# Kernel tuning notes

Hardware: AMD Instinct MI355X
Metric: run time of the kernel (lower is better)

Reference implementation:

```python
import jax, jax.numpy as jnp
import numpy as np


def setup_inputs() -> dict:
    key = jax.random.key(0)
    ks = jax.random.split(key, 9)
    B, L, D, H, E = 8, 2048, 1024, 256, 8
    Hg = D // 4
    s = 0.02
    return {
        "x": jax.random.normal(ks[0], (B, L, D), dtype=jnp.float32),
        "wg1": jax.random.normal(ks[1], (D, Hg), dtype=jnp.float32) * s,
        "bg1": jax.random.normal(ks[2], (Hg,), dtype=jnp.float32) * s,
        "wg2": jax.random.normal(ks[3], (Hg, E), dtype=jnp.float32) * s,
        "bg2": jax.random.normal(ks[4], (E,), dtype=jnp.float32) * s,
        "w1": jax.random.normal(ks[5], (E, D, H), dtype=jnp.float32) * (1.0 / np.sqrt(D)),
        "b1": jax.random.normal(ks[6], (E, H), dtype=jnp.float32) * s,
        "w2": jax.random.normal(ks[7], (E, H, D), dtype=jnp.float32) * (1.0 / np.sqrt(H)),
        "b2": jax.random.normal(ks[8], (E, D), dtype=jnp.float32) * s,
        "k": 2,
    }


def reference(x, wg1, bg1, wg2, bg2, w1, b1, w2, b2, k):
    B, L, D = x.shape
    xt = x.reshape(-1, D)                       # [T, D] tokens
    T = xt.shape[0]
    # gating MLP: Linear -> GELU(exact, matches torch nn.GELU) -> Linear -> softmax
    logits = jax.nn.gelu(xt @ wg1 + bg1, approximate=False) @ wg2 + bg2  # [T, E]
    scores = jax.nn.softmax(logits, axis=-1)
    top_v, top_i = jax.lax.top_k(scores, k)     # [T, k]
    # dense gate matrix (equivalent to compute_gating's scatter); zeros for non-top-k
    gates = jnp.zeros_like(scores).at[jnp.arange(T)[:, None], top_i].set(top_v)  # [T, E]

    # grouped-GEMM MoE: y[t] = sum_e gates[t,e] * (gelu(x[t] @ W1_e + b1_e) @ W2_e + b2_e)
    # scan over the fixed, small expert axis; gates zero out non-selected experts,
    # giving math identical to the sort/dispatch + per-expert torch.mm loop.
    def body(acc, we):
        w1e, b1e, w2e, b2e, ge = we
        h = jax.nn.gelu(xt @ w1e + b1e, approximate=False)  # [T, H]
        o = h @ w2e + b2e                                    # [T, D]
        return acc + ge[:, None] * o, None

    y, _ = jax.lax.scan(body, jnp.zeros_like(xt), (w1, b1, w2, b2, gates.T))
    return y.reshape(B, L, D)
```

## Files before the change

kernel.cpp:

```cpp
#include <hip/hip_runtime.h>

typedef unsigned short u16;
typedef __attribute__((ext_vector_type(8))) short bf16x8;
typedef __attribute__((ext_vector_type(4))) float f32x4;
typedef __attribute__((ext_vector_type(4))) u16 u16x4;

#define T_TOK 16384
#define D_DIM 1024
#define NE 8
#define MAXP 33792

__device__ __forceinline__ u16 f2bf(float f) {
  union { float f; unsigned int u; } c; c.f = f;
  unsigned int u = c.u;
  u += 0x7fffu + ((u >> 16) & 1u);
  return (u16)(u >> 16);
}

__device__ __forceinline__ float bf2f(u16 v) {
  union { unsigned int u; float f; } c; c.u = ((unsigned int)v) << 16;
  return c.f;
}

__device__ __forceinline__ float gelu_exact(float u) {
  return 0.5f * u * (1.0f + erff(u * 0.70710678118654752f));
}

__device__ __forceinline__ void gld16(const void* g, void* l) {
  __builtin_amdgcn_global_load_lds(
      (const __attribute__((address_space(1))) unsigned int*)g,
      (__attribute__((address_space(3))) unsigned int*)l, 16, 0, 0);
}

__device__ __forceinline__ void stage_tile(u16* lds, const char* g0, size_t stride,
                                           int wid, int lane) {
  const char* g = g0 + (size_t)(wid * 8 + (lane >> 3)) * stride + (size_t)((lane & 7) * 16);
  char* l = (char*)lds + wid * 1024;
  #pragma unroll
  for (int c = 0; c < 4; ++c)
    gld16(g + (size_t)(32 * c) * stride, l + c * 4096);
}

__device__ __forceinline__ void stage_b32(u16* lds, const u16* mat, int rowbase,
                                          int k0, int wid, int lane) {
  const char* g0 = (const char*)(mat + (size_t)rowbase * 1024 + k0);
  #pragma unroll
  for (int c = 0; c < 2; ++c) {
    const int row = c * 64 + wid * 16 + (lane >> 2);
    const char* g = g0 + (size_t)row * 2048 + (size_t)((lane & 3) * 16);
    char* l = (char*)lds + c * 4096 + wid * 1024;
    gld16(g, l);
  }
}

__device__ __forceinline__ void mma_step(const u16* As, const u16* Bs, f32x4 acc[4][4],
                                         int wm, int wn, int lane) {
  const int r = lane & 15, kq = (lane >> 4) * 8;
  #pragma unroll
  for (int ks = 0; ks < 2; ++ks) {
    const int col = ks * 32 + kq;
    bf16x8 a[4], b[4];
    #pragma unroll
    for (int mf = 0; mf < 4; ++mf)
      a[mf] = *(const bf16x8*)&As[(wm * 64 + mf * 16 + r) * 64 + col];
    #pragma unroll
    for (int nf = 0; nf < 4; ++nf)
      b[nf] = *(const bf16x8*)&Bs[(wn * 64 + nf * 16 + r) * 64 + col];
    #pragma unroll
    for (int mf = 0; mf < 4; ++mf)
      #pragma unroll
      for (int nf = 0; nf < 4; ++nf)
        acc[mf][nf] = __builtin_amdgcn_mfma_f32_16x16x32_bf16(a[mf], b[nf], acc[mf][nf], 0, 0, 0);
  }
}

__global__ __launch_bounds__(256) void transpose_cvt_kernel(const float* __restrict__ in,
                                                            u16* __restrict__ out,
                                                            int R, int C) {
  __shared__ u16 t[32][36];
  const int e = blockIdx.z;
  const int r0 = blockIdx.x * 32, c0 = blockIdx.y * 32;
  const int tid = threadIdx.x;
  {
    const int r = tid >> 3, cq = (tid & 7) * 4;
    float4 v = *(const float4*)(in + ((size_t)e * R + r0 + r) * C + c0 + cq);
    t[r][cq + 0] = f2bf(v.x); t[r][cq + 1] = f2bf(v.y);
    t[r][cq + 2] = f2bf(v.z); t[r][cq + 3] = f2bf(v.w);
  }
  __syncthreads();
  {
    const int c = tid >> 3, rq = (tid & 7) * 4;
    u16x4 o;
    o.x = t[rq + 0][c]; o.y = t[rq + 1][c]; o.z = t[rq + 2][c]; o.w = t[rq + 3][c];
    *(u16x4*)(out + ((size_t)e * C + c0 + c) * R + r0 + rq) = o;
  }
}

__global__ __launch_bounds__(256) void transpose_hilo_kernel(const float* __restrict__ in,
                                                             u16* __restrict__ out_hi,
                                                             u16* __restrict__ out_lo,
                                                             int R, int C) {
  __shared__ u16 th[32][36];
  __shared__ u16 tl[32][36];
  const int r0 = blockIdx.x * 32, c0 = blockIdx.y * 32;
  const int tid = threadIdx.x;
  {
    const int r = tid >> 3, cq = (tid & 7) * 4;
    float4 v = *(const float4*)(in + (size_t)(r0 + r) * C + c0 + cq);
    float vv[4] = {v.x, v.y, v.z, v.w};
    #pragma unroll
    for (int i = 0; i < 4; ++i) {
      u16 h = f2bf(vv[i]);
      th[r][cq + i] = h;
      tl[r][cq + i] = f2bf(vv[i] - bf2f(h));
    }
  }
  __syncthreads();
  {
    const int c = tid >> 3, rq = (tid & 7) * 4;
    u16x4 oh, ol;
    oh.x = th[rq + 0][c]; oh.y = th[rq + 1][c]; oh.z = th[rq + 2][c]; oh.w = th[rq + 3][c];
    ol.x = tl[rq + 0][c]; ol.y = tl[rq + 1][c]; ol.z = tl[rq + 2][c]; ol.w = tl[rq + 3][c];
    *(u16x4*)(out_hi + (size_t)(c0 + c) * R + r0 + rq) = oh;
    *(u16x4*)(out_lo + (size_t)(c0 + c) * R + r0 + rq) = ol;
  }
}

__global__ __launch_bounds__(256) void gating_mfma_kernel(
    const float* __restrict__ x, const u16* __restrict__ wg1t_hi,
    const u16* __restrict__ wg1t_lo, u16* __restrict__ xb,
    float* __restrict__ p_buf) {
  __shared__ u16 Ah[2][128 * 32], Al[2][128 * 32];
  __shared__ u16 Bh[2][128 * 32], Bl[2][128 * 32];
  const int tid = threadIdx.x, lane = tid & 63, wid = tid >> 6;
  const int t0 = blockIdx.x * 128, n0 = blockIdx.y * 128;
  const int wm = wid >> 1, wn = wid & 1;
  const bool emit = (blockIdx.y == 0);
  const int arow = tid >> 1, akb = (tid & 1) * 16;

  f32x4 acc[4][4];
  #pragma unroll
  for (int i = 0; i < 4; ++i)
    #pragma unroll
    for (int j = 0; j < 4; ++j) acc[i][j] = (f32x4){0.f, 0.f, 0.f, 0.f};

  stage_b32(Bh[0], wg1t_hi, n0, 0, wid, lane);
  stage_b32(Bl[0], wg1t_lo, n0, 0, wid, lane);
  {
    const float* src = x + (size_t)(t0 + arow) * 1024 + akb;
    #pragma unroll
    for (int i = 0; i < 4; ++i) {
      float4 v = *(const float4*)(src + i * 4);
      float vv[4] = {v.x, v.y, v.z, v.w};
      u16x4 h, l;
      u16 hh[4], ll[4];
      #pragma unroll
      for (int q = 0; q < 4; ++q) { hh[q] = f2bf(vv[q]); ll[q] = f2bf(vv[q] - bf2f(hh[q])); }
      h.x = hh[0]; h.y = hh[1]; h.z = hh[2]; h.w = hh[3];
      l.x = ll[0]; l.y = ll[1]; l.z = ll[2]; l.w = ll[3];
      *(u16x4*)&Ah[0][arow * 32 + akb + i * 4] = h;
      *(u16x4*)&Al[0][arow * 32 + akb + i * 4] = l;
      if (emit) *(u16x4*)(xb + (size_t)(t0 + arow) * 1024 + akb + i * 4) = h;
    }
  }
  __syncthreads();

  int cur = 0;
  for (int kt = 0; kt < 32; ++kt) {
    const bool has_next = kt < 31;
    const int nxt = cur ^ 1;
    float4 xv[4];
    if (has_next) {
      stage_b32(Bh[nxt], wg1t_hi, n0, (kt + 1) * 32, wid, lane);
      stage_b32(Bl[nxt], wg1t_lo, n0, (kt + 1) * 32, wid, lane);
      const float* src = x + (size_t)(t0 + arow) * 1024 + (kt + 1) * 32 + akb;
      #pragma unroll
      for (int i = 0; i < 4; ++i) xv[i] = *(const float4*)(src + i * 4);
    }
    {
      const int r = lane & 15, kq = (lane >> 4) * 8;
      bf16x8 ah[4], al[4], bh[4], bl[4];
      #pragma unroll
      for (int mf = 0; mf < 4; ++mf) {
        const int ro = (wm * 64 + mf * 16 + r) * 32 + kq;
        ah[mf] = *(const bf16x8*)&Ah[cur][ro];
        al[mf] = *(const bf16x8*)&Al[cur][ro];
      }
      #pragma unroll
      for (int nf = 0; nf < 4; ++nf) {
        const int ro = (wn * 64 + nf * 16 + r) * 32 + kq;
        bh[nf] = *(const bf16x8*)&Bh[cur][ro];
        bl[nf] = *(const bf16x8*)&Bl[cur][ro];
      }
      #pragma unroll
      for (int mf = 0; mf < 4; ++mf)
        #pragma unroll
        for (int nf = 0; nf < 4; ++nf) {
          acc[mf][nf] = __builtin_amdgcn_mfma_f32_16x16x32_bf16(ah[mf], bh[nf], acc[mf][nf], 0, 0, 0);
          acc[mf][nf] = __builtin_amdgcn_mfma_f32_16x16x32_bf16(ah[mf], bl[nf], acc[mf][nf], 0, 0, 0);
          acc[mf][nf] = __builtin_amdgcn_mfma_f32_16x16x32_bf16(al[mf], bh[nf], acc[mf][nf], 0, 0, 0);
        }
    }
    if (has_next) {
      #pragma unroll
      for (int i = 0; i < 4; ++i) {
        float vv[4] = {xv[i].x, xv[i].y, xv[i].z, xv[i].w};
        u16x4 h, l;
        u16 hh[4], ll[4];
        #pragma unroll
        for (int q = 0; q < 4; ++q) { hh[q] = f2bf(vv[q]); ll[q] = f2bf(vv[q] - bf2f(hh[q])); }
        h.x = hh[0]; h.y = hh[1]; h.z = hh[2]; h.w = hh[3];
        l.x = ll[0]; l.y = ll[1]; l.z = ll[2]; l.w = ll[3];
        *(u16x4*)&Ah[nxt][arow * 32 + akb + i * 4] = h;
        *(u16x4*)&Al[nxt][arow * 32 + akb + i * 4] = l;
        if (emit) *(u16x4*)(xb + (size_t)(t0 + arow) * 1024 + (kt + 1) * 32 + akb + i * 4) = h;
      }
    }
    __syncthreads();
    cur ^= 1;
  }

  #pragma unroll
  for (int mf = 0; mf < 4; ++mf)
    #pragma unroll
    for (int rr = 0; rr < 4; ++rr) {
      const int lt = wm * 64 + mf * 16 + ((lane >> 4) << 2) + rr;
      #pragma unroll
      for (int nf = 0; nf < 4; ++nf) {
        const int ln = wn * 64 + nf * 16 + (lane & 15);
        p_buf[(size_t)(t0 + lt) * 256 + n0 + ln] = acc[mf][nf][rr];
      }
    }
}

__global__ __launch_bounds__(256) void gating_p2_kernel(
    const float* __restrict__ p_buf, const float* __restrict__ bg1,
    const float* __restrict__ wg2, const float* __restrict__ bg2,
    int* __restrict__ top_i, float2* __restrict__ top_g) {
  const int tid = threadIdx.x;
  const int tn = tid & 31, tm = tid >> 5;
  const int t0 = blockIdx.x * 32;

  float bb[8];
  {
    float4 ba = *(const float4*)&bg1[tn * 4];
    float4 bc = *(const float4*)&bg1[128 + tn * 4];
    bb[0] = ba.x; bb[1] = ba.y; bb[2] = ba.z; bb[3] = ba.w;
    bb[4] = bc.x; bb[5] = bc.y; bb[6] = bc.z; bb[7] = bc.w;
  }

  float hv[4][8];
  #pragma unroll
  for (int i = 0; i < 4; ++i) {
    const size_t t = t0 + tm * 4 + i;
    const float* p = &p_buf[t * 256];
    float4 a0 = *(const float4*)&p[tn * 4];
    float4 a1 = *(const float4*)&p[128 + tn * 4];
    hv[i][0] = gelu_exact(a0.x + bb[0]);
    hv[i][1] = gelu_exact(a0.y + bb[1]);
    hv[i][2] = gelu_exact(a0.z + bb[2]);
    hv[i][3] = gelu_exact(a0.w + bb[3]);
    hv[i][4] = gelu_exact(a1.x + bb[4]);
    hv[i][5] = gelu_exact(a1.y + bb[5]);
    hv[i][6] = gelu_exact(a1.z + bb[6]);
    hv[i][7] = gelu_exact(a1.w + bb[7]);
  }

  float part[4][8];
  #pragma unroll
  for (int i = 0; i < 4; ++i)
    #pragma unroll
    for (int e = 0; e < 8; ++e) part[i][e] = 0.f;
  #pragma unroll
  for (int j = 0; j < 8; ++j) {
    const int col = (j < 4) ? (tn * 4 + j) : (128 + tn * 4 + (j - 4));
    float4 wa = *(const float4*)&wg2[col * 8];
    float4 wb = *(const float4*)&wg2[col * 8 + 4];
    float we[8] = {wa.x, wa.y, wa.z, wa.w, wb.x, wb.y, wb.z, wb.w};
    #pragma unroll
    for (int i = 0; i < 4; ++i)
      #pragma unroll
      for (int e = 0; e < 8; ++e) part[i][e] += hv[i][j] * we[e];
  }
  #pragma unroll
  for (int mask = 1; mask < 32; mask <<= 1)
    #pragma unroll
    for (int i = 0; i < 4; ++i)
      #pragma unroll
      for (int e = 0; e < 8; ++e) part[i][e] += __shfl_xor(part[i][e], mask);

  if (tn < 4) {
    float lg[8];
    #pragma unroll
    for (int i = 0; i < 4; ++i)
      if (tn == i) {
        #pragma unroll
        for (int e = 0; e < 8; ++e) lg[e] = part[i][e];
      }
    #pragma unroll
    for (int e = 0; e < 8; ++e) lg[e] += bg2[e];
    float m = lg[0];
    #pragma unroll
    for (int e = 1; e < 8; ++e) m = fmaxf(m, lg[e]);
    float ex[8], s = 0.f;
    #pragma unroll
    for (int e = 0; e < 8; ++e) { ex[e] = expf(lg[e] - m); s += ex[e]; }
    int i1 = 0;
    #pragma unroll
    for (int e = 1; e < 8; ++e) if (lg[e] > lg[i1]) i1 = e;
    int i2 = (i1 == 0) ? 1 : 0;
    #pragma unroll
    for (int e = 0; e < 8; ++e) if (e != i1 && lg[e] > lg[i2]) i2 = e;
    float inv = 1.f / s;
    const int t = t0 + tm * 4 + tn;
    top_i[t] = i1 | (i2 << 8);
    top_g[t] = make_float2(ex[i1] * inv, ex[i2] * inv);
  }
}

__global__ __launch_bounds__(256) void hist_kernel(const int* __restrict__ top_i,
                                                   int* __restrict__ hist) {
  __shared__ int h[NE];
  const int tid = threadIdx.x;
  if (tid < NE) h[tid] = 0;
  __syncthreads();
  const int ti = top_i[blockIdx.x * 256 + tid];
  atomicAdd(&h[ti & 255], 1);
  atomicAdd(&h[ti >> 8], 1);
  __syncthreads();
  if (tid < NE) hist[blockIdx.x * NE + tid] = h[tid];
}

__global__ __launch_bounds__(64) void scan_kernel(const int* __restrict__ hist,
                                                  int* __restrict__ cnt,
                                                  int* __restrict__ offs,
                                                  int* __restrict__ cbase) {
  __shared__ int tot[NE], off_s[NE];
  const int tid = threadIdx.x;
  if (tid < NE) {
    int s = 0;
    for (int c = 0; c < 64; ++c) s += hist[c * NE + tid];
    tot[tid] = s; cnt[tid] = s;
  }
  __syncthreads();
  if (tid == 0) {
    int o = 0;
    #pragma unroll
    for (int e = 0; e < NE; ++e) { off_s[e] = o; o += (tot[e] + 127) & ~127; }
  }
  __syncthreads();
  if (tid < NE) {
    offs[tid] = off_s[tid];
    int r = off_s[tid];
    for (int c = 0; c < 64; ++c) { cbase[c * NE + tid] = r; r += hist[c * NE + tid]; }
  }
}

__global__ __launch_bounds__(256) void fill_kernel(
    const int* __restrict__ top_i, const int* __restrict__ cbase,
    int* __restrict__ tok_list, int* __restrict__ pos1, int* __restrict__ pos2) {
  __shared__ int lcnt[NE];
  const int tid = threadIdx.x;
  if (tid < NE) lcnt[tid] = 0;
  __syncthreads();
  const int t = blockIdx.x * 256 + tid;
  const int ti = top_i[t];
  const int i1 = ti & 255, i2 = ti >> 8;
  const int r1 = atomicAdd(&lcnt[i1], 1);
  const int r2 = atomicAdd(&lcnt[i2], 1);
  const int p1 = cbase[blockIdx.x * NE + i1] + r1;
  const int p2 = cbase[blockIdx.x * NE + i2] + r2;
  tok_list[p1] = t; tok_list[p2] = t;
  pos1[t] = p1; pos2[t] = p2;
}

__global__ __launch_bounds__(256) void expert_h_kernel(
    const u16* __restrict__ xb, const u16* __restrict__ w1t,
    const float* __restrict__ b1, const int* __restrict__ tok_list,
    const int* __restrict__ cnt, const int* __restrict__ offs,
    u16* __restrict__ h_c) {
  __shared__ u16 As[128 * 64];
  __shared__ u16 Bs[128 * 64];
  __shared__ float b1_s[128];
  const int e = blockIdx.z;
  const int nblk = (cnt[e] + 127) >> 7;
  if ((int)blockIdx.x >= nblk) return;
  const int tid = threadIdx.x, lane = tid & 63, wid = tid >> 6;
  const int base = offs[e] + blockIdx.x * 128;
  const int n0 = blockIdx.y * 128;
  const int wm = wid >> 1, wn = wid & 1;

  if (tid < 128) b1_s[tid] = b1[e * 256 + n0 + tid];

  int tk[4];
  {
    const int r0 = wid * 8 + (lane >> 3);
    #pragma unroll
    for (int c = 0; c < 4; ++c) tk[c] = tok_list[base + r0 + 32 * c];
  }

  f32x4 acc[4][4];
  #pragma unroll
  for (int i = 0; i < 4; ++i)
    #pragma unroll
    for (int j = 0; j < 4; ++j) acc[i][j] = (f32x4){0.f, 0.f, 0.f, 0.f};

  const char* Bb = (const char*)w1t + ((size_t)e * 256 + n0) * 2048;
  const int cb = (lane & 7) * 16;
  for (int kt = 0; kt < 16; ++kt) {
    __syncthreads();
    {
      char* l = (char*)As + wid * 1024;
      #pragma unroll
      for (int c = 0; c < 4; ++c)
        gld16((const char*)xb + (size_t)tk[c] * 2048 + kt * 128 + cb, l + c * 4096);
    }
    stage_tile(Bs, Bb + kt * 128, 2048, wid, lane);
    __syncthreads();
    mma_step(As, Bs, acc, wm, wn, lane);
  }

  #pragma unroll
  for (int mf = 0; mf < 4; ++mf)
    #pragma unroll
    for (int rr = 0; rr < 4; ++rr) {
      const int lt = wm * 64 + mf * 16 + ((lane >> 4) << 2) + rr;
      #pragma unroll
      for (int nf = 0; nf < 4; ++nf) {
        const int ln = wn * 64 + nf * 16 + (lane & 15);
        float u = acc[mf][nf][rr] + b1_s[ln];
        h_c[(size_t)(base + lt) * 256 + n0 + ln] = f2bf(gelu_exact(u));
      }
    }
}

__global__ __launch_bounds__(256) void moe_out_kernel(
    const u16* __restrict__ h_c, const u16* __restrict__ w2t,
    const float* __restrict__ b2, const int* __restrict__ cnt,
    const int* __restrict__ offs, u16* __restrict__ o_c) {
  __shared__ u16 As[128 * 64];
  __shared__ u16 Bs[128 * 64];
  __shared__ float b2_s[128];
  const int e = blockIdx.z;
  const int nblk = (cnt[e] + 127) >> 7;
  if ((int)blockIdx.x >= nblk) return;
  const int tid = threadIdx.x, lane = tid & 63, wid = tid >> 6;
  const int base = offs[e] + blockIdx.x * 128;
  const int n0 = blockIdx.y * 128;
  const int wm = wid >> 1, wn = wid & 1;

  if (tid < 128) b2_s[tid] = b2[(size_t)e * 1024 + n0 + tid];

  f32x4 acc[4][4];
  #pragma unroll
  for (int i = 0; i < 4; ++i)
    #pragma unroll
    for (int j = 0; j < 4; ++j) acc[i][j] = (f32x4){0.f, 0.f, 0.f, 0.f};

  const char* Ab = (const char*)h_c + (size_t)base * 512;
  const char* Bb = (const char*)w2t + ((size_t)e * D_DIM + n0) * 512;
  #pragma unroll 1
  for (int kt = 0; kt < 4; ++kt) {
    __syncthreads();
    stage_tile(As, Ab + kt * 128, 512, wid, lane);
    stage_tile(Bs, Bb + kt * 128, 512, wid, lane);
    __syncthreads();
    mma_step(As, Bs, acc, wm, wn, lane);
  }

  #pragma unroll
  for (int mf = 0; mf < 4; ++mf)
    #pragma unroll
    for (int rr = 0; rr < 4; ++rr) {
      const int lt = wm * 64 + mf * 16 + ((lane >> 4) << 2) + rr;
      #pragma unroll
      for (int nf = 0; nf < 4; ++nf) {
        const int ln = wn * 64 + nf * 16 + (lane & 15);
        o_c[(size_t)(base + lt) * 1024 + n0 + ln] = f2bf(acc[mf][nf][rr] + b2_s[ln]);
      }
    }
}

__global__ __launch_bounds__(256) void gather_kernel(
    const u16* __restrict__ o_c, const int* __restrict__ pos1,
    const int* __restrict__ pos2, const float2* __restrict__ top_g,
    float* __restrict__ y) {
  const int t = blockIdx.x;
  const int p1 = pos1[t], p2 = pos2[t];
  const float2 g = top_g[t];
  const int c = threadIdx.x * 4;
  u16x4 a = *(const u16x4*)&o_c[(size_t)p1 * 1024 + c];
  u16x4 b = *(const u16x4*)&o_c[(size_t)p2 * 1024 + c];
  float4 o;
  o.x = g.x * bf2f(a.x) + g.y * bf2f(b.x);
  o.y = g.x * bf2f(a.y) + g.y * bf2f(b.y);
  o.z = g.x * bf2f(a.z) + g.y * bf2f(b.z);
  o.w = g.x * bf2f(a.w) + g.y * bf2f(b.w);
  *(float4*)&y[(size_t)t * 1024 + c] = o;
}

extern "C" void kernel_launch(void* const* d_in, const int* in_sizes, int n_in,
                              void* d_out, int out_size, void* d_ws, size_t ws_size,
                              hipStream_t stream) {
  (void)in_sizes; (void)n_in; (void)out_size; (void)ws_size;
  const float* x   = (const float*)d_in[0];
  const float* wg1 = (const float*)d_in[1];
  const float* bg1 = (const float*)d_in[2];
  const float* wg2 = (const float*)d_in[3];
  const float* bg2 = (const float*)d_in[4];
  const float* w1  = (const float*)d_in[5];
  const float* b1  = (const float*)d_in[6];
  const float* w2  = (const float*)d_in[7];
  const float* b2  = (const float*)d_in[8];
  float* y = (float*)d_out;

  char* ws = (char*)d_ws;
  u16* xb   = (u16*)(ws);
  u16* w1t  = (u16*)(ws + 33554432);
  u16* w2t  = (u16*)(ws + 37748736);
  char* M   = ws + 41943040;
  int*    cnt      = (int*)(M);
  int*    offs     = (int*)(M + 64);
  int*    hist     = (int*)(M + 128);
  int*    cbase    = (int*)(M + 2304);
  int*    tok_list = (int*)(M + 4608);
  int*    top_i    = (int*)(M + 139776);
  float2* top_g    = (float2*)(M + 205312);
  int*    pos1     = (int*)(M + 336384);
  int*    pos2     = (int*)(M + 401920);
  u16* h_c = (u16*)(ws + 42467328);
  u16* o_c = (u16*)(ws + 59768832);
  float* p_buf   = (float*)(ws + 59768832);
  u16*   wg1t_hi = (u16*)(ws + 59768832 + 16777216);
  u16*   wg1t_lo = (u16*)(ws + 59768832 + 17301504);

  hipMemsetAsync(tok_list, 0, 135168, stream);
  transpose_cvt_kernel<<<dim3(32, 8, 8), 256, 0, stream>>>(w1, w1t, 1024, 256);
  transpose_cvt_kernel<<<dim3(8, 32, 8), 256, 0, stream>>>(w2, w2t, 256, 1024);
  transpose_hilo_kernel<<<dim3(32, 8), 256, 0, stream>>>(wg1, wg1t_hi, wg1t_lo, 1024, 256);
  gating_mfma_kernel<<<dim3(128, 2), 256, 0, stream>>>(x, wg1t_hi, wg1t_lo, xb, p_buf);
  gating_p2_kernel<<<512, 256, 0, stream>>>(p_buf, bg1, wg2, bg2, top_i, top_g);
  hist_kernel<<<64, 256, 0, stream>>>(top_i, hist);
  scan_kernel<<<1, 64, 0, stream>>>(hist, cnt, offs, cbase);
  fill_kernel<<<64, 256, 0, stream>>>(top_i, cbase, tok_list, pos1, pos2);
  expert_h_kernel<<<dim3(128, 2, 8), 256, 0, stream>>>(xb, w1t, b1, tok_list, cnt, offs, h_c);
  moe_out_kernel <<<dim3(128, 8, 8), 256, 0, stream>>>(h_c, w2t, b2, cnt, offs, o_c);
  gather_kernel  <<<16384, 256, 0, stream>>>(o_c, pos1, pos2, top_g, y);
}
```

Baseline: 208.5 us.

## Split gating GEMM over K halves and shrink expert_h M-tile to 64

The gating GEMM now runs on a grid with a z dimension of two, each block reducing half of the 1024-long K axis and writing its own partial p_buf slab. gating_p2 sums the two partials before adding the bias and applying GELU. expert_h_kernel moves from 128-token to 64-token M tiles and launches twice as many blocks per expert. Both changes raise block count and occupancy on the many CUs, at the cost of extra p_buf traffic and less reuse of each B tile.

Measured after the change: 189.2 us. 1.1x faster.

```diff
diff --git a/kernel.cpp b/kernel.cpp
--- a/kernel.cpp
+++ b/kernel.cpp
@@ -134,6 +134,7 @@
   __shared__ u16 Bh[2][128 * 32], Bl[2][128 * 32];
   const int tid = threadIdx.x, lane = tid & 63, wid = tid >> 6;
   const int t0 = blockIdx.x * 128, n0 = blockIdx.y * 128;
+  const int kh = blockIdx.z, kbeg = kh * 512;
   const int wm = wid >> 1, wn = wid & 1;
   const bool emit = (blockIdx.y == 0);
   const int arow = tid >> 1, akb = (tid & 1) * 16;
@@ -144,10 +145,10 @@
     #pragma unroll
     for (int j = 0; j < 4; ++j) acc[i][j] = (f32x4){0.f, 0.f, 0.f, 0.f};
 
-  stage_b32(Bh[0], wg1t_hi, n0, 0, wid, lane);
-  stage_b32(Bl[0], wg1t_lo, n0, 0, wid, lane);
+  stage_b32(Bh[0], wg1t_hi, n0, kbeg, wid, lane);
+  stage_b32(Bl[0], wg1t_lo, n0, kbeg, wid, lane);
   {
-    const float* src = x + (size_t)(t0 + arow) * 1024 + akb;
+    const float* src = x + (size_t)(t0 + arow) * 1024 + kbeg + akb;
     #pragma unroll
     for (int i = 0; i < 4; ++i) {
       float4 v = *(const float4*)(src + i * 4);
@@ -160,20 +161,20 @@
       l.x = ll[0]; l.y = ll[1]; l.z = ll[2]; l.w = ll[3];
       *(u16x4*)&Ah[0][arow * 32 + akb + i * 4] = h;
       *(u16x4*)&Al[0][arow * 32 + akb + i * 4] = l;
-      if (emit) *(u16x4*)(xb + (size_t)(t0 + arow) * 1024 + akb + i * 4) = h;
+      if (emit) *(u16x4*)(xb + (size_t)(t0 + arow) * 1024 + kbeg + akb + i * 4) = h;
     }
   }
   __syncthreads();
 
   int cur = 0;
-  for (int kt = 0; kt < 32; ++kt) {
-    const bool has_next = kt < 31;
+  for (int kt = 0; kt < 16; ++kt) {
+    const bool has_next = kt < 15;
     const int nxt = cur ^ 1;
     float4 xv[4];
     if (has_next) {
-      stage_b32(Bh[nxt], wg1t_hi, n0, (kt + 1) * 32, wid, lane);
-      stage_b32(Bl[nxt], wg1t_lo, n0, (kt + 1) * 32, wid, lane);
-      const float* src = x + (size_t)(t0 + arow) * 1024 + (kt + 1) * 32 + akb;
+      stage_b32(Bh[nxt], wg1t_hi, n0, kbeg + (kt + 1) * 32, wid, lane);
+      stage_b32(Bl[nxt], wg1t_lo, n0, kbeg + (kt + 1) * 32, wid, lane);
+      const float* src = x + (size_t)(t0 + arow) * 1024 + kbeg + (kt + 1) * 32 + akb;
       #pragma unroll
       for (int i = 0; i < 4; ++i) xv[i] = *(const float4*)(src + i * 4);
     }
@@ -213,7 +214,8 @@
         l.x = ll[0]; l.y = ll[1]; l.z = ll[2]; l.w = ll[3];
         *(u16x4*)&Ah[nxt][arow * 32 + akb + i * 4] = h;
         *(u16x4*)&Al[nxt][arow * 32 + akb + i * 4] = l;
-        if (emit) *(u16x4*)(xb + (size_t)(t0 + arow) * 1024 + (kt + 1) * 32 + akb + i * 4) = h;
+        if (emit)
+          *(u16x4*)(xb + (size_t)(t0 + arow) * 1024 + kbeg + (kt + 1) * 32 + akb + i * 4) = h;
       }
     }
     __syncthreads();
@@ -228,7 +230,7 @@
       #pragma unroll
       for (int nf = 0; nf < 4; ++nf) {
         const int ln = wn * 64 + nf * 16 + (lane & 15);
-        p_buf[(size_t)(t0 + lt) * 256 + n0 + ln] = acc[mf][nf][rr];
+        p_buf[((size_t)kh * T_TOK + t0 + lt) * 256 + n0 + ln] = acc[mf][nf][rr];
       }
     }
 }
@@ -253,17 +255,20 @@
   #pragma unroll
   for (int i = 0; i < 4; ++i) {
     const size_t t = t0 + tm * 4 + i;
-    const float* p = &p_buf[t * 256];
-    float4 a0 = *(const float4*)&p[tn * 4];
-    float4 a1 = *(const float4*)&p[128 + tn * 4];
-    hv[i][0] = gelu_exact(a0.x + bb[0]);
-    hv[i][1] = gelu_exact(a0.y + bb[1]);
-    hv[i][2] = gelu_exact(a0.z + bb[2]);
-    hv[i][3] = gelu_exact(a0.w + bb[3]);
-    hv[i][4] = gelu_exact(a1.x + bb[4]);
-    hv[i][5] = gelu_exact(a1.y + bb[5]);
-    hv[i][6] = gelu_exact(a1.z + bb[6]);
-    hv[i][7] = gelu_exact(a1.w + bb[7]);
+    const float* pa = &p_buf[t * 256];
+    const float* pb = &p_buf[((size_t)T_TOK + t) * 256];
+    float4 a0 = *(const float4*)&pa[tn * 4];
+    float4 a1 = *(const float4*)&pa[128 + tn * 4];
+    float4 b0 = *(const float4*)&pb[tn * 4];
+    float4 b1 = *(const float4*)&pb[128 + tn * 4];
+    hv[i][0] = gelu_exact(a0.x + b0.x + bb[0]);
+    hv[i][1] = gelu_exact(a0.y + b0.y + bb[1]);
+    hv[i][2] = gelu_exact(a0.z + b0.z + bb[2]);
+    hv[i][3] = gelu_exact(a0.w + b0.w + bb[3]);
+    hv[i][4] = gelu_exact(a1.x + b1.x + bb[4]);
+    hv[i][5] = gelu_exact(a1.y + b1.y + bb[5]);
+    hv[i][6] = gelu_exact(a1.z + b1.z + bb[6]);
+    hv[i][7] = gelu_exact(a1.w + b1.w + bb[7]);
   }
 
   float part[4][8];
@@ -379,29 +384,27 @@
     const float* __restrict__ b1, const int* __restrict__ tok_list,
     const int* __restrict__ cnt, const int* __restrict__ offs,
     u16* __restrict__ h_c) {
-  __shared__ u16 As[128 * 64];
+  __shared__ u16 As[64 * 64];
   __shared__ u16 Bs[128 * 64];
   __shared__ float b1_s[128];
   const int e = blockIdx.z;
-  const int nblk = (cnt[e] + 127) >> 7;
+  const int nblk = (cnt[e] + 63) >> 6;
   if ((int)blockIdx.x >= nblk) return;
   const int tid = threadIdx.x, lane = tid & 63, wid = tid >> 6;
-  const int base = offs[e] + blockIdx.x * 128;
+  const int base = offs[e] + blockIdx.x * 64;
   const int n0 = blockIdx.y * 128;
   const int wm = wid >> 1, wn = wid & 1;
 
   if (tid < 128) b1_s[tid] = b1[e * 256 + n0 + tid];
 
-  int tk[4];
-  {
-    const int r0 = wid * 8 + (lane >> 3);
-    #pragma unroll
-    for (int c = 0; c < 4; ++c) tk[c] = tok_list[base + r0 + 32 * c];
-  }
-
-  f32x4 acc[4][4];
-  #pragma unroll
-  for (int i = 0; i < 4; ++i)
+  int tk[2];
+  #pragma unroll
+  for (int c = 0; c < 2; ++c)
+    tk[c] = tok_list[base + (wid * 2 + c) * 8 + (lane >> 3)];
+
+  f32x4 acc[2][4];
+  #pragma unroll
+  for (int i = 0; i < 2; ++i)
     #pragma unroll
     for (int j = 0; j < 4; ++j) acc[i][j] = (f32x4){0.f, 0.f, 0.f, 0.f};
 
@@ -410,21 +413,39 @@
   for (int kt = 0; kt < 16; ++kt) {
     __syncthreads();
     {
-      char* l = (char*)As + wid * 1024;
-      #pragma unroll
-      for (int c = 0; c < 4; ++c)
-        gld16((const char*)xb + (size_t)tk[c] * 2048 + kt * 128 + cb, l + c * 4096);
+      char* l = (char*)As + wid * 2048;
+      #pragma unroll
+      for (int c = 0; c < 2; ++c)
+        gld16((const char*)xb + (size_t)tk[c] * 2048 + kt * 128 + cb, l + c * 1024);
     }
     stage_tile(Bs, Bb + kt * 128, 2048, wid, lane);
     __syncthreads();
-    mma_step(As, Bs, acc, wm, wn, lane);
-  }
-
-  #pragma unroll
-  for (int mf = 0; mf < 4; ++mf)
+    {
+      const int r = lane & 15, kq = (lane >> 4) * 8;
+      #pragma unroll
+      for (int ks = 0; ks < 2; ++ks) {
+        const int col = ks * 32 + kq;
+        bf16x8 a[2], b[4];
+        #pragma unroll
+        for (int mf = 0; mf < 2; ++mf)
+          a[mf] = *(const bf16x8*)&As[(wm * 32 + mf * 16 + r) * 64 + col];
+        #pragma unroll
+        for (int nf = 0; nf < 4; ++nf)
+          b[nf] = *(const bf16x8*)&Bs[(wn * 64 + nf * 16 + r) * 64 + col];
+        #pragma unroll
+        for (int mf = 0; mf < 2; ++mf)
+          #pragma unroll
+          for (int nf = 0; nf < 4; ++nf)
+            acc[mf][nf] = __builtin_amdgcn_mfma_f32_16x16x32_bf16(a[mf], b[nf], acc[mf][nf], 0, 0, 0);
+      }
+    }
+  }
+
+  #pragma unroll
+  for (int mf = 0; mf < 2; ++mf)
     #pragma unroll
     for (int rr = 0; rr < 4; ++rr) {
-      const int lt = wm * 64 + mf * 16 + ((lane >> 4) << 2) + rr;
+      const int lt = wm * 32 + mf * 16 + ((lane >> 4) << 2) + rr;
       #pragma unroll
       for (int nf = 0; nf < 4; ++nf) {
         const int ln = wn * 64 + nf * 16 + (lane & 15);
@@ -531,19 +552,19 @@
   u16* h_c = (u16*)(ws + 42467328);
   u16* o_c = (u16*)(ws + 59768832);
   float* p_buf   = (float*)(ws + 59768832);
-  u16*   wg1t_hi = (u16*)(ws + 59768832 + 16777216);
-  u16*   wg1t_lo = (u16*)(ws + 59768832 + 17301504);
+  u16*   wg1t_hi = (u16*)(ws + 93323264);
+  u16*   wg1t_lo = (u16*)(ws + 93847552);
 
   hipMemsetAsync(tok_list, 0, 135168, stream);
   transpose_cvt_kernel<<<dim3(32, 8, 8), 256, 0, stream>>>(w1, w1t, 1024, 256);
   transpose_cvt_kernel<<<dim3(8, 32, 8), 256, 0, stream>>>(w2, w2t, 256, 1024);
   transpose_hilo_kernel<<<dim3(32, 8), 256, 0, stream>>>(wg1, wg1t_hi, wg1t_lo, 1024, 256);
-  gating_mfma_kernel<<<dim3(128, 2), 256, 0, stream>>>(x, wg1t_hi, wg1t_lo, xb, p_buf);
+  gating_mfma_kernel<<<dim3(128, 2, 2), 256, 0, stream>>>(x, wg1t_hi, wg1t_lo, xb, p_buf);
   gating_p2_kernel<<<512, 256, 0, stream>>>(p_buf, bg1, wg2, bg2, top_i, top_g);
   hist_kernel<<<64, 256, 0, stream>>>(top_i, hist);
   scan_kernel<<<1, 64, 0, stream>>>(hist, cnt, offs, cbase);
   fill_kernel<<<64, 256, 0, stream>>>(top_i, cbase, tok_list, pos1, pos2);
-  expert_h_kernel<<<dim3(128, 2, 8), 256, 0, stream>>>(xb, w1t, b1, tok_list, cnt, offs, h_c);
+  expert_h_kernel<<<dim3(256, 2, 8), 256, 0, stream>>>(xb, w1t, b1, tok_list, cnt, offs, h_c);
   moe_out_kernel <<<dim3(128, 8, 8), 256, 0, stream>>>(h_c, w2t, b2, cnt, offs, o_c);
   gather_kernel  <<<16384, 256, 0, stream>>>(o_c, pos1, pos2, top_g, y);
 }
```
